# Optimization experiments

Hardware: AMD Instinct MI355X
Metric: run time of the kernel (lower is better)

Reference implementation:

```python
import jax, jax.numpy as jnp
import numpy as np

B, L, D_MODEL = 2, 2048, 2048
N_HEADS, N_GROUPS = 16, 4
D_HEAD = D_MODEL // N_HEADS  # 128
H_DIM = 5632
EPS = 1e-6


def rmsnorm(x, g):
    var = jnp.mean(x * x, axis=-1, keepdims=True)
    return x * jax.lax.rsqrt(var + EPS) * g


def apply_rope(x):
    # x: [b, H, l, d_head]; interleaved even/odd rotation as in the source
    l, d_head = x.shape[2], x.shape[3]
    pos = jnp.arange(l, dtype=jnp.float32)[:, None]                      # [l,1]
    div = 10000.0 ** (jnp.arange(0, d_head, 2, dtype=jnp.float32) / d_head)
    cos_e = jnp.cos(pos / div)                                           # [l, d_head//2]
    sin_e = jnp.sin(pos / div)
    xe, xo = x[..., 0::2], x[..., 1::2]
    re = xe * cos_e - xo * sin_e
    ro = xe * sin_e + xo * cos_e
    return jnp.stack([re, ro], axis=-1).reshape(x.shape)


def gqa_attention(q, k, v):
    # q: [b,l,d_model], k/v: [b,l,n_groups*d_head]
    b, l, _ = q.shape
    # faithful to source: direct contiguous view, NO transpose
    q = q.reshape(b, N_HEADS, l, D_HEAD)
    k = k.reshape(b, N_GROUPS, l, D_HEAD)
    v = v.reshape(b, N_GROUPS, l, D_HEAD)
    q = apply_rope(q)
    k = apply_rope(k)
    hpg = N_HEADS // N_GROUPS
    qg = q.reshape(b, N_GROUPS, hpg, l, D_HEAD)
    scale = 1.0 / jnp.sqrt(jnp.asarray(D_HEAD, dtype=q.dtype))
    scores = jnp.einsum('bghqd,bgkd->bghqk', qg, k) * scale              # [b,g,hpg,l,l]
    causal = jnp.tril(jnp.ones((l, l), dtype=bool))
    scores = jnp.where(causal, scores, jnp.asarray(-jnp.inf, scores.dtype))
    p = jax.nn.softmax(scores, axis=-1)
    out = jnp.einsum('bghqk,bgkd->bghqd', p, v)                          # [b,g,hpg,l,d]
    return out.reshape(b, N_HEADS, l, D_HEAD).reshape(b, l, D_MODEL)


def setup_inputs() -> dict:
    key = jax.random.key(0)
    ks = jax.random.split(key, 10)
    s_d = 1.0 / np.sqrt(D_MODEL)
    s_h = 1.0 / np.sqrt(H_DIM)
    return {
        'x': jax.random.normal(ks[0], (B, L, D_MODEL), jnp.float32),
        'g1': jnp.ones((D_MODEL,), jnp.float32),
        'wq': jax.random.normal(ks[1], (D_MODEL, D_MODEL), jnp.float32) * s_d,
        'bq': jnp.zeros((D_MODEL,), jnp.float32),
        'wk': jax.random.normal(ks[2], (D_MODEL, N_GROUPS * D_HEAD), jnp.float32) * s_d,
        'bk': jnp.zeros((N_GROUPS * D_HEAD,), jnp.float32),
        'wv': jax.random.normal(ks[3], (D_MODEL, N_GROUPS * D_HEAD), jnp.float32) * s_d,
        'bv': jnp.zeros((N_GROUPS * D_HEAD,), jnp.float32),
        'wo': jax.random.normal(ks[4], (D_MODEL, D_MODEL), jnp.float32) * s_d,
        'bo': jnp.zeros((D_MODEL,), jnp.float32),
        'g2': jnp.ones((D_MODEL,), jnp.float32),
        'w1': jax.random.normal(ks[5], (D_MODEL, H_DIM), jnp.float32) * s_d,
        'b1': jnp.zeros((H_DIM,), jnp.float32),
        'wg': jax.random.normal(ks[6], (D_MODEL, H_DIM), jnp.float32) * s_d,
        'bg': jnp.zeros((H_DIM,), jnp.float32),
        'w2': jax.random.normal(ks[7], (H_DIM, D_MODEL), jnp.float32) * s_h,
        'b2': jnp.zeros((D_MODEL,), jnp.float32),
    }


def reference(x, g1, wq, bq, wk, bk, wv, bv, wo, bo, g2, w1, b1, wg, bg, w2, b2):
    # pre-norm GQA attention block
    h = rmsnorm(x, g1)
    q = h @ wq + bq
    k = h @ wk + bk
    v = h @ wv + bv
    attn = gqa_attention(q, k, v)
    x = x + attn @ wo + bo
    # pre-norm SwiGLU FFN
    h2 = rmsnorm(x, g2)
    ffn = (jax.nn.silu(h2 @ w1 + b1) * (h2 @ wg + bg)) @ w2 + b2
    return x + ffn
```

## Files before the change

### kernel.cpp

```cpp
#include <hip/hip_runtime.h>
#include <math.h>

#define BATCH 2
#define SEQ 2048
#define DM 2048
#define NH 16
#define NG 4
#define DH 128
#define HDIM 5632
#define MROWS (BATCH * SEQ)
#define KVD (NG * DH)

typedef __attribute__((ext_vector_type(8))) short short8;
typedef __attribute__((ext_vector_type(4))) float f32x4;
typedef __attribute__((ext_vector_type(4))) unsigned short us4;
typedef unsigned short ushortT;

__device__ __forceinline__ unsigned short f2bf(float x) {
  unsigned int u = __float_as_uint(x);
  u += 0x7FFFu + ((u >> 16) & 1u);
  return (unsigned short)(u >> 16);
}
__device__ __forceinline__ float bf2f(unsigned short h) {
  return __uint_as_float(((unsigned int)h) << 16);
}

__global__ __launch_bounds__(256) void rmsnorm_planes(
    const float* __restrict__ x, const float* __restrict__ g,
    ushortT* __restrict__ Ah, ushortT* __restrict__ Al) {
  int row = blockIdx.x;
  const float4* xr = (const float4*)(x + (size_t)row * DM);
  const float4* g4 = (const float4*)g;
  int t = threadIdx.x;
  float4 a = xr[t];
  float4 b = xr[t + 256];
  float ss = a.x * a.x + a.y * a.y + a.z * a.z + a.w * a.w +
             b.x * b.x + b.y * b.y + b.z * b.z + b.w * b.w;
#pragma unroll
  for (int off = 32; off > 0; off >>= 1) ss += __shfl_xor(ss, off);
  __shared__ float red[4];
  if ((t & 63) == 0) red[t >> 6] = ss;
  __syncthreads();
  float tot = red[0] + red[1] + red[2] + red[3];
  float inv = rsqrtf(tot * (1.0f / DM) + 1e-6f);
  float4 ga = g4[t], gb = g4[t + 256];
  float va[4] = {a.x * inv * ga.x, a.y * inv * ga.y, a.z * inv * ga.z,
                 a.w * inv * ga.w};
  float vb[4] = {b.x * inv * gb.x, b.y * inv * gb.y, b.z * inv * gb.z,
                 b.w * inv * gb.w};
  us4 ha, la, hb, lb;
#pragma unroll
  for (int i = 0; i < 4; i++) {
    ushortT h = f2bf(va[i]);
    ha[i] = h; la[i] = f2bf(va[i] - bf2f(h));
    h = f2bf(vb[i]);
    hb[i] = h; lb[i] = f2bf(vb[i] - bf2f(h));
  }
  size_t o = (size_t)row * DM + 4 * t;
  *(us4*)&Ah[o] = ha; *(us4*)&Al[o] = la;
  *(us4*)&Ah[o + 1024] = hb; *(us4*)&Al[o + 1024] = lb;
}

__global__ __launch_bounds__(256) void split_wt(
    const float* __restrict__ W, ushortT* __restrict__ Wth,
    ushortT* __restrict__ Wtl, int K, int N) {
  __shared__ float Ls[64][65];
  int t = threadIdx.x;
  int nb = blockIdx.x * 64, kb = blockIdx.y * 64;
  int lr = t >> 4, lc = (t & 15) * 4;
#pragma unroll
  for (int r = 0; r < 4; r++) {
    float4 v = *(const float4*)&W[(size_t)(kb + lr + r * 16) * N + nb + lc];
    Ls[lr + r * 16][lc + 0] = v.x;
    Ls[lr + r * 16][lc + 1] = v.y;
    Ls[lr + r * 16][lc + 2] = v.z;
    Ls[lr + r * 16][lc + 3] = v.w;
  }
  __syncthreads();
  int nr = t >> 2, kc = (t & 3) * 16;
  ushortT hv[16], lv[16];
#pragma unroll
  for (int i = 0; i < 16; i++) {
    float v = Ls[kc + i][nr];
    hv[i] = f2bf(v);
    lv[i] = f2bf(v - bf2f(hv[i]));
  }
  size_t o = (size_t)(nb + nr) * K + kb + kc;
  *(uint4*)&Wth[o] = *(uint4*)&hv[0];
  *(uint4*)&Wth[o + 8] = *(uint4*)&hv[8];
  *(uint4*)&Wtl[o] = *(uint4*)&lv[0];
  *(uint4*)&Wtl[o + 8] = *(uint4*)&lv[8];
}

template <int EPI>
__global__ __launch_bounds__(256) void gemm_pl(
    const ushortT* __restrict__ Ah, const ushortT* __restrict__ Al,
    const ushortT* __restrict__ Wth, const ushortT* __restrict__ Wtl,
    const float* __restrict__ bias, const float* __restrict__ auxf,
    const ushortT* __restrict__ auxh, const ushortT* __restrict__ auxl,
    float* __restrict__ Cf, ushortT* __restrict__ Ch,
    ushortT* __restrict__ Cl, int M, int N, int K) {
  __shared__ ushortT As[2][128][40];
  __shared__ ushortT Bs[2][128][40];
  int t = threadIdx.x;
  int lane = t & 63, wid = t >> 6;
  int wr = wid >> 1, wc = wid & 1;
  int row0 = blockIdx.y * 128, col0 = blockIdx.x * 128;

  f32x4 acc[4][4];
#pragma unroll
  for (int mi = 0; mi < 4; mi++)
#pragma unroll
    for (int ni = 0; ni < 4; ni++)
#pragma unroll
      for (int j = 0; j < 4; j++) acc[mi][ni][j] = 0.f;

  int am = t >> 1, ak = (t & 1) * 16;
  int bn = t & 127, bk = (t >> 7) * 16;
  int fr = lane & 15, fq = lane >> 4;
  int fk = fq * 8;

  const ushortT* a0 = Ah + (size_t)(row0 + am) * K + ak;
  const ushortT* a1 = Al + (size_t)(row0 + am) * K + ak;
  const ushortT* b0 = Wth + (size_t)(col0 + bn) * K + bk;
  const ushortT* b1 = Wtl + (size_t)(col0 + bn) * K + bk;

  uint4 ra0 = *(const uint4*)(a0), ra1 = *(const uint4*)(a0 + 8);
  uint4 ra2 = *(const uint4*)(a1), ra3 = *(const uint4*)(a1 + 8);
  uint4 rb0 = *(const uint4*)(b0), rb1 = *(const uint4*)(b0 + 8);
  uint4 rb2 = *(const uint4*)(b1), rb3 = *(const uint4*)(b1 + 8);

  for (int k0 = 0; k0 < K; k0 += 32) {
    __syncthreads();
    *(uint4*)&As[0][am][ak + 0] = ra0;
    *(uint4*)&As[0][am][ak + 8] = ra1;
    *(uint4*)&As[1][am][ak + 0] = ra2;
    *(uint4*)&As[1][am][ak + 8] = ra3;
    *(uint4*)&Bs[0][bn][bk + 0] = rb0;
    *(uint4*)&Bs[0][bn][bk + 8] = rb1;
    *(uint4*)&Bs[1][bn][bk + 0] = rb2;
    *(uint4*)&Bs[1][bn][bk + 8] = rb3;
    __syncthreads();

    if (k0 + 32 < K) {
      ra0 = *(const uint4*)(a0 + k0 + 32);
      ra1 = *(const uint4*)(a0 + k0 + 40);
      ra2 = *(const uint4*)(a1 + k0 + 32);
      ra3 = *(const uint4*)(a1 + k0 + 40);
      rb0 = *(const uint4*)(b0 + k0 + 32);
      rb1 = *(const uint4*)(b0 + k0 + 40);
      rb2 = *(const uint4*)(b1 + k0 + 32);
      rb3 = *(const uint4*)(b1 + k0 + 40);
    }

    short8 bfr[4][2];
#pragma unroll
    for (int ni = 0; ni < 4; ni++) {
      int brow = wc * 64 + ni * 16 + fr;
      bfr[ni][0] = *(const short8*)&Bs[0][brow][fk];
      bfr[ni][1] = *(const short8*)&Bs[1][brow][fk];
    }
#pragma unroll
    for (int mi = 0; mi < 4; mi++) {
      int arow = wr * 64 + mi * 16 + fr;
      short8 a_h = *(const short8*)&As[0][arow][fk];
      short8 a_l = *(const short8*)&As[1][arow][fk];
#pragma unroll
      for (int ni = 0; ni < 4; ni++) {
        acc[mi][ni] = __builtin_amdgcn_mfma_f32_16x16x32_bf16(
            a_h, bfr[ni][0], acc[mi][ni], 0, 0, 0);
        acc[mi][ni] = __builtin_amdgcn_mfma_f32_16x16x32_bf16(
            a_h, bfr[ni][1], acc[mi][ni], 0, 0, 0);
        acc[mi][ni] = __builtin_amdgcn_mfma_f32_16x16x32_bf16(
            a_l, bfr[ni][0], acc[mi][ni], 0, 0, 0);
      }
    }
  }

#pragma unroll
  for (int mi = 0; mi < 4; mi++) {
#pragma unroll
    for (int ni = 0; ni < 4; ni++) {
      int row = row0 + wr * 64 + mi * 16 + fq * 4;
      int col = col0 + wc * 64 + ni * 16 + fr;
      float bc = bias[col];
#pragma unroll
      for (int j = 0; j < 4; j++) {
        size_t idx = (size_t)(row + j) * N + col;
        float v = acc[mi][ni][j] + bc;
        if (EPI == 1) v += auxf[idx];
        if (EPI == 3) {
          float u = bf2f(auxh[idx]) + bf2f(auxl[idx]);
          v = v * (u / (1.f + expf(-u)));
        }
        if (EPI <= 1) {
          Cf[idx] = v;
        } else {
          ushortT h = f2bf(v);
          Ch[idx] = h;
          Cl[idx] = f2bf(v - bf2f(h));
        }
      }
    }
  }
}

__global__ __launch_bounds__(256) void rope_table_kernel(float* __restrict__ tab) {
  int idx = blockIdx.x * 256 + threadIdx.x;
  if (idx >= SEQ * 64) return;
  int l = idx >> 6, i = idx & 63;
  double div = pow(10000.0, (double)(2 * i) / (double)DH);
  double ang = (double)l / div;
  tab[idx * 2 + 0] = (float)cos(ang);
  tab[idx * 2 + 1] = (float)sin(ang);
}

__global__ __launch_bounds__(256) void gather_rope_q_bf(
    const float* __restrict__ qmat, const float* __restrict__ tab,
    ushortT* __restrict__ Qh, ushortT* __restrict__ Ql) {
  int gid = blockIdx.x * 4 + (threadIdx.x >> 6);
  int lane = threadIdx.x & 63;
  int b = gid >> 15;
  int rem = gid & 32767;
  int h = rem >> 11, l2 = rem & 2047;
  int srow = h * 128 + (l2 >> 4);
  int scol = (l2 & 15) * 128;
  const float2* src = (const float2*)(qmat + ((size_t)b * SEQ + srow) * DM + scol);
  float2 v = src[lane];
  float2 cs = ((const float2*)tab)[l2 * 64 + lane];
  const float scale = (float)(0.08838834764831845 * 1.4426950408889634);
  float ox = (v.x * cs.x - v.y * cs.y) * scale;
  float oy = (v.x * cs.y + v.y * cs.x) * scale;
  ushortT hx = f2bf(ox), hy = f2bf(oy);
  ushortT lx = f2bf(ox - bf2f(hx)), ly = f2bf(oy - bf2f(hy));
  size_t o = (size_t)gid * DH + 2 * lane;
  Qh[o] = hx; Qh[o + 1] = hy;
  Ql[o] = lx; Ql[o + 1] = ly;
}

__global__ __launch_bounds__(256) void gather_k_bf(
    const float* __restrict__ mat, const float* __restrict__ tab,
    ushortT* __restrict__ Kh, ushortT* __restrict__ Kl) {
  int gid = blockIdx.x * 4 + (threadIdx.x >> 6);
  int lane = threadIdx.x & 63;
  int b = gid >> 13;
  int rem = gid & 8191;
  int g = rem >> 11, l2 = rem & 2047;
  int srow = g * 512 + (l2 >> 2);
  int scol = (l2 & 3) * 128;
  const float2* src = (const float2*)(mat + ((size_t)b * SEQ + srow) * KVD + scol);
  float2 v = src[lane];
  float2 cs = ((const float2*)tab)[l2 * 64 + lane];
  float ox = v.x * cs.x - v.y * cs.y;
  float oy = v.x * cs.y + v.y * cs.x;
  ushortT hx = f2bf(ox), hy = f2bf(oy);
  ushortT lx = f2bf(ox - bf2f(hx)), ly = f2bf(oy - bf2f(hy));
  size_t o = (size_t)gid * DH + 2 * lane;
  Kh[o] = hx; Kh[o + 1] = hy;
  Kl[o] = lx; Kl[o + 1] = ly;
}

__global__ __launch_bounds__(256) void gather_vt_bf(
    const float* __restrict__ vmat, ushortT* __restrict__ Vth,
    ushortT* __restrict__ Vtl) {
  __shared__ float Ls[64][33];
  int t = threadIdx.x;
  int bg = blockIdx.z;
  int b = bg >> 2, g = bg & 3;
  int l2base = blockIdx.x * 64, dbase = blockIdx.y * 32;
  int l2 = l2base + (t >> 2);
  int srow = g * 512 + (l2 >> 2);
  int scol = (l2 & 3) * 128 + dbase + (t & 3) * 8;
  const float* src = vmat + ((size_t)b * SEQ + srow) * KVD + scol;
  float4 v0 = *(const float4*)src;
  float4 v1 = *(const float4*)(src + 4);
  int lr = t >> 2, lc = (t & 3) * 8;
  Ls[lr][lc + 0] = v0.x; Ls[lr][lc + 1] = v0.y;
  Ls[lr][lc + 2] = v0.z; Ls[lr][lc + 3] = v0.w;
  Ls[lr][lc + 4] = v1.x; Ls[lr][lc + 5] = v1.y;
  Ls[lr][lc + 6] = v1.z; Ls[lr][lc + 7] = v1.w;
  __syncthreads();
  short8 hv, lv;
#pragma unroll
  for (int i = 0; i < 8; i++) {
    float v = Ls[(t & 7) * 8 + i][t >> 3];
    unsigned short h = f2bf(v);
    hv[i] = (short)h;
    lv[i] = (short)f2bf(v - bf2f(h));
  }
  size_t o = ((size_t)bg * DH + dbase + (t >> 3)) * SEQ + l2base + (t & 7) * 8;
  *(short8*)(Vth + o) = hv;
  *(short8*)(Vtl + o) = lv;
}

__global__ __launch_bounds__(256) void attn_mfma(
    const ushortT* __restrict__ Qh, const ushortT* __restrict__ Ql,
    const ushortT* __restrict__ Kh, const ushortT* __restrict__ Kl,
    const ushortT* __restrict__ Vth, const ushortT* __restrict__ Vtl,
    float* __restrict__ O) {
  __shared__ ushortT Ks[2][32][136];
  __shared__ ushortT Vts[2][128][40];
  __shared__ ushortT Ps[4][16][40];
  int t = threadIdx.x;
  int lane = t & 63, w = t >> 6;
  int fr = lane & 15, fq = lane >> 4;
  int bh = blockIdx.y;
  int bg = (bh >> 4) * NG + ((bh & 15) >> 2);
  int q0 = ((int)gridDim.x - 1 - (int)blockIdx.x) * 64;

  short8 qfh[4], qfl[4];
  {
    const ushortT* qs = Qh + ((size_t)bh * SEQ + q0 + w * 16 + fr) * DH + fq * 8;
    const ushortT* qs2 = Ql + ((size_t)bh * SEQ + q0 + w * 16 + fr) * DH + fq * 8;
#pragma unroll
    for (int ks = 0; ks < 4; ks++) {
      qfh[ks] = *(const short8*)(qs + ks * 32);
      qfl[ks] = *(const short8*)(qs2 + ks * 32);
    }
  }

  f32x4 oacc[8];
#pragma unroll
  for (int nt = 0; nt < 8; nt++)
#pragma unroll
    for (int j = 0; j < 4; j++) oacc[nt][j] = 0.f;
  float m[4], l[4];
#pragma unroll
  for (int j = 0; j < 4; j++) { m[j] = -INFINITY; l[j] = 0.f; }

  int nkt = q0 / 32 + 2;
  for (int kt = 0; kt < nkt; kt++) {
    int p = t >> 7, tt = t & 127;
    int kr = tt >> 2, cb = (tt & 3) * 32;
    const ushortT* ksp =
        (p ? Kl : Kh) + ((size_t)bg * SEQ + kt * 32 + kr) * DH + cb;
    uint4 k0 = *(const uint4*)(ksp + 0), k1 = *(const uint4*)(ksp + 8);
    uint4 k2 = *(const uint4*)(ksp + 16), k3 = *(const uint4*)(ksp + 24);
    const ushortT* vsp = (p ? Vtl : Vth) + ((size_t)bg * DH + tt) * SEQ + kt * 32;
    uint4 v0 = *(const uint4*)(vsp + 0), v1 = *(const uint4*)(vsp + 8);
    uint4 v2 = *(const uint4*)(vsp + 16), v3 = *(const uint4*)(vsp + 24);

    __syncthreads();
    *(uint4*)&Ks[p][kr][cb + 0] = k0;
    *(uint4*)&Ks[p][kr][cb + 8] = k1;
    *(uint4*)&Ks[p][kr][cb + 16] = k2;
    *(uint4*)&Ks[p][kr][cb + 24] = k3;
    int xs = (tt & 3) << 3;
    *(uint4*)&Vts[p][tt][0 ^ xs] = v0;
    *(uint4*)&Vts[p][tt][8 ^ xs] = v1;
    *(uint4*)&Vts[p][tt][16 ^ xs] = v2;
    *(uint4*)&Vts[p][tt][24 ^ xs] = v3;
    __syncthreads();

    f32x4 sc[2];
#pragma unroll
    for (int ct = 0; ct < 2; ct++)
#pragma unroll
      for (int j = 0; j < 4; j++) sc[ct][j] = 0.f;
#pragma unroll
    for (int ct = 0; ct < 2; ct++)
#pragma unroll
      for (int ks = 0; ks < 4; ks++) {
        short8 kfh = *(const short8*)&Ks[0][ct * 16 + fr][ks * 32 + fq * 8];
        short8 kfl = *(const short8*)&Ks[1][ct * 16 + fr][ks * 32 + fq * 8];
        sc[ct] = __builtin_amdgcn_mfma_f32_16x16x32_bf16(qfh[ks], kfh, sc[ct], 0, 0, 0);
        sc[ct] = __builtin_amdgcn_mfma_f32_16x16x32_bf16(qfh[ks], kfl, sc[ct], 0, 0, 0);
        sc[ct] = __builtin_amdgcn_mfma_f32_16x16x32_bf16(qfl[ks], kfh, sc[ct], 0, 0, 0);
      }

    float alpha[4];
#pragma unroll
    for (int j = 0; j < 4; j++) {
      int qg = q0 + w * 16 + fq * 4 + j;
      float s0 = (kt * 32 + fr <= qg) ? sc[0][j] : -INFINITY;
      float s1 = (kt * 32 + 16 + fr <= qg) ? sc[1][j] : -INFINITY;
      float mx = fmaxf(s0, s1);
      mx = fmaxf(mx, __shfl_xor(mx, 1));
      mx = fmaxf(mx, __shfl_xor(mx, 2));
      mx = fmaxf(mx, __shfl_xor(mx, 4));
      mx = fmaxf(mx, __shfl_xor(mx, 8));
      float mn = fmaxf(m[j], mx);
      float al = exp2f(m[j] - mn);
      float p0 = exp2f(s0 - mn), p1 = exp2f(s1 - mn);
      float rs = p0 + p1;
      rs += __shfl_xor(rs, 1);
      rs += __shfl_xor(rs, 2);
      rs += __shfl_xor(rs, 4);
      rs += __shfl_xor(rs, 8);
      l[j] = l[j] * al + rs;
      m[j] = mn;
      alpha[j] = al;
      Ps[w][fq * 4 + j][fr] = f2bf(p0);
      Ps[w][fq * 4 + j][16 + fr] = f2bf(p1);
    }
#pragma unroll
    for (int nt = 0; nt < 8; nt++) {
      oacc[nt][0] *= alpha[0];
      oacc[nt][1] *= alpha[1];
      oacc[nt][2] *= alpha[2];
      oacc[nt][3] *= alpha[3];
    }

    short8 pah = *(const short8*)&Ps[w][fr][fq * 8];
#pragma unroll
    for (int nt = 0; nt < 8; nt++) {
      int vr = nt * 16 + fr;
      int vc = (fq * 8) ^ ((fr & 3) << 3);
      short8 vfh = *(const short8*)&Vts[0][vr][vc];
      short8 vfl = *(const short8*)&Vts[1][vr][vc];
      oacc[nt] = __builtin_amdgcn_mfma_f32_16x16x32_bf16(pah, vfh, oacc[nt], 0, 0, 0);
      oacc[nt] = __builtin_amdgcn_mfma_f32_16x16x32_bf16(pah, vfl, oacc[nt], 0, 0, 0);
    }
  }

  float inv[4];
#pragma unroll
  for (int j = 0; j < 4; j++) inv[j] = 1.f / l[j];
  float* ob = O + ((size_t)bh * SEQ + q0 + w * 16 + fq * 4) * DH + fr;
#pragma unroll
  for (int nt = 0; nt < 8; nt++)
#pragma unroll
    for (int j = 0; j < 4; j++)
      ob[(size_t)j * DH + nt * 16] = oacc[nt][j] * inv[j];
}

__global__ __launch_bounds__(256) void scatter_o_planes(
    const float* __restrict__ O, ushortT* __restrict__ Sh,
    ushortT* __restrict__ Sl) {
  size_t i4 = (size_t)blockIdx.x * 256 + threadIdx.x;
  size_t f = i4 * 4;
  int b = (int)(f >> 22);
  int rem = (int)(f & 4194303);
  int l = rem >> 11, d = rem & 2047;
  int c = l * 16 + (d >> 7);
  int h = c >> 11, l2 = c & 2047, d2 = d & 127;
  float4 v = *(const float4*)&O[(((size_t)b * NH + h) * SEQ + l2) * DH + d2];
  float vv[4] = {v.x, v.y, v.z, v.w};
  us4 hv, lv;
#pragma unroll
  for (int i = 0; i < 4; i++) {
    ushortT h16 = f2bf(vv[i]);
    hv[i] = h16;
    lv[i] = f2bf(vv[i] - bf2f(h16));
  }
  *(us4*)&Sh[f] = hv;
  *(us4*)&Sl[f] = lv;
}

extern "C" void kernel_launch(void* const* d_in, const int* in_sizes, int n_in,
                              void* d_out, int out_size, void* d_ws,
                              size_t ws_size, hipStream_t stream) {
  if (ws_size < 53739520ull * 4ull) return;

  const float* x  = (const float*)d_in[0];
  const float* g1 = (const float*)d_in[1];
  const float* wq = (const float*)d_in[2];
  const float* bq = (const float*)d_in[3];
  const float* wk = (const float*)d_in[4];
  const float* bk = (const float*)d_in[5];
  const float* wv = (const float*)d_in[6];
  const float* bv = (const float*)d_in[7];
  const float* wo = (const float*)d_in[8];
  const float* bo = (const float*)d_in[9];
  const float* g2 = (const float*)d_in[10];
  const float* w1 = (const float*)d_in[11];
  const float* b1 = (const float*)d_in[12];
  const float* wg = (const float*)d_in[13];
  const float* bg = (const float*)d_in[14];
  const float* w2 = (const float*)d_in[15];
  const float* b2 = (const float*)d_in[16];
  float* out = (float*)d_out;
  float* ws = (float*)d_ws;

  ushortT* WTh = (ushortT*)(ws + 0);
  ushortT* Hh  = (ushortT*)(ws + 11534336);
  ushortT* Hl  = Hh + 8388608;
  float* qmat  = ws + 19922944;
  float* kmat  = ws + 28311552;
  float* vmat  = ws + 30408704;
  ushortT* Qh  = (ushortT*)(ws + 32505856);
  ushortT* Ql  = Qh + 8388608;
  ushortT* Kh  = (ushortT*)(ws + 40894464);
  ushortT* Kl  = Kh + 2097152;
  ushortT* Vth = (ushortT*)(ws + 42991616);
  ushortT* Vtl = Vth + 2097152;
  float* x2    = ws + 45088768;
  float* tab   = ws + 53477376;
  float* O     = qmat;
  ushortT* Sh  = Qh;
  ushortT* Sl  = Sh + 8388608;
  ushortT* Uh  = (ushortT*)qmat;
  ushortT* Ul  = Uh + 23068672;

  rope_table_kernel<<<(SEQ * 64 + 255) / 256, 256, 0, stream>>>(tab);
  rmsnorm_planes<<<MROWS, 256, 0, stream>>>(x, g1, Hh, Hl);

  split_wt<<<dim3(DM / 64, DM / 64), 256, 0, stream>>>(wq, WTh, WTh + DM * DM, DM, DM);
  gemm_pl<0><<<dim3(DM / 128, MROWS / 128), 256, 0, stream>>>(
      Hh, Hl, WTh, WTh + DM * DM, bq, nullptr, nullptr, nullptr, qmat, nullptr,
      nullptr, MROWS, DM, DM);
  split_wt<<<dim3(KVD / 64, DM / 64), 256, 0, stream>>>(wk, WTh, WTh + DM * KVD, DM, KVD);
  gemm_pl<0><<<dim3(KVD / 128, MROWS / 128), 256, 0, stream>>>(
      Hh, Hl, WTh, WTh + DM * KVD, bk, nullptr, nullptr, nullptr, kmat, nullptr,
      nullptr, MROWS, KVD, DM);
  split_wt<<<dim3(KVD / 64, DM / 64), 256, 0, stream>>>(wv, WTh, WTh + DM * KVD, DM, KVD);
  gemm_pl<0><<<dim3(KVD / 128, MROWS / 128), 256, 0, stream>>>(
      Hh, Hl, WTh, WTh + DM * KVD, bv, nullptr, nullptr, nullptr, vmat, nullptr,
      nullptr, MROWS, KVD, DM);

  gather_rope_q_bf<<<(BATCH * NH * SEQ) / 4, 256, 0, stream>>>(qmat, tab, Qh, Ql);
  gather_k_bf<<<(BATCH * NG * SEQ) / 4, 256, 0, stream>>>(kmat, tab, Kh, Kl);
  gather_vt_bf<<<dim3(SEQ / 64, DH / 32, BATCH * NG), 256, 0, stream>>>(vmat, Vth, Vtl);

  attn_mfma<<<dim3(SEQ / 64, BATCH * NH), 256, 0, stream>>>(Qh, Ql, Kh, Kl,
                                                            Vth, Vtl, O);
  scatter_o_planes<<<(MROWS * DM / 4) / 256, 256, 0, stream>>>(O, Sh, Sl);

  split_wt<<<dim3(DM / 64, DM / 64), 256, 0, stream>>>(wo, WTh, WTh + DM * DM, DM, DM);
  gemm_pl<1><<<dim3(DM / 128, MROWS / 128), 256, 0, stream>>>(
      Sh, Sl, WTh, WTh + DM * DM, bo, x, nullptr, nullptr, x2, nullptr,
      nullptr, MROWS, DM, DM);

  rmsnorm_planes<<<MROWS, 256, 0, stream>>>(x2, g2, Hh, Hl);

  split_wt<<<dim3(HDIM / 64, DM / 64), 256, 0, stream>>>(w1, WTh, WTh + DM * HDIM, DM, HDIM);
  gemm_pl<2><<<dim3(HDIM / 128, MROWS / 128), 256, 0, stream>>>(
      Hh, Hl, WTh, WTh + DM * HDIM, b1, nullptr, nullptr, nullptr, nullptr, Uh,
      Ul, MROWS, HDIM, DM);
  split_wt<<<dim3(HDIM / 64, DM / 64), 256, 0, stream>>>(wg, WTh, WTh + DM * HDIM, DM, HDIM);
  gemm_pl<3><<<dim3(HDIM / 128, MROWS / 128), 256, 0, stream>>>(
      Hh, Hl, WTh, WTh + DM * HDIM, bg, nullptr, Uh, Ul, nullptr, Uh, Ul,
      MROWS, HDIM, DM);

  split_wt<<<dim3(DM / 64, HDIM / 64), 256, 0, stream>>>(w2, WTh, WTh + HDIM * DM, HDIM, DM);
  gemm_pl<1><<<dim3(DM / 128, MROWS / 128), 256, 0, stream>>>(
      Uh, Ul, WTh, WTh + HDIM * DM, b2, x2, nullptr, nullptr, out, nullptr,
      nullptr, MROWS, DM, HDIM);
}
```

Baseline: 2.026 ms.

## Fuse QKV projections, merge SwiGLU GEMMs, prefetch K/V tiles in attention

The three Q/K/V projection GEMMs become one GEMM over concatenated transposed weights and a concatenated bias, and the gather kernels read from the combined output. The two FFN up and gate GEMMs become a single 512-thread kernel that computes both accumulators per tile and applies SiLU-gating in its epilogue. This avoids writing and rereading the intermediate U planes and saves several launches. The attention loop now loads the next K/V tile into registers while the current tile is in use, and the residual x2 is kept in the output buffer. In exchange the workspace grows, register pressure rises in the dual GEMM and in attention, and the final residual add reads and writes the same buffer in place.

```diff
diff --git a/kernel.cpp b/kernel.cpp
--- a/kernel.cpp
+++ b/kernel.cpp
@@ -10,6 +10,7 @@
 #define HDIM 5632
 #define MROWS (BATCH * SEQ)
 #define KVD (NG * DH)
+#define QKVD 3072
 
 typedef __attribute__((ext_vector_type(8))) short short8;
 typedef __attribute__((ext_vector_type(4))) float f32x4;
@@ -92,14 +93,20 @@
   *(uint4*)&Wtl[o + 8] = *(uint4*)&lv[8];
 }
 
+__global__ __launch_bounds__(256) void bias_cat(
+    const float* __restrict__ bq, const float* __restrict__ bk,
+    const float* __restrict__ bv, float* __restrict__ dst) {
+  int t = blockIdx.x * 256 + threadIdx.x;
+  if (t >= QKVD) return;
+  dst[t] = (t < DM) ? bq[t] : ((t < DM + KVD) ? bk[t - DM] : bv[t - DM - KVD]);
+}
+
 template <int EPI>
 __global__ __launch_bounds__(256) void gemm_pl(
     const ushortT* __restrict__ Ah, const ushortT* __restrict__ Al,
     const ushortT* __restrict__ Wth, const ushortT* __restrict__ Wtl,
     const float* __restrict__ bias, const float* __restrict__ auxf,
-    const ushortT* __restrict__ auxh, const ushortT* __restrict__ auxl,
-    float* __restrict__ Cf, ushortT* __restrict__ Ch,
-    ushortT* __restrict__ Cl, int M, int N, int K) {
+    float* __restrict__ Cf, int M, int N, int K) {
   __shared__ ushortT As[2][128][40];
   __shared__ ushortT Bs[2][128][40];
   int t = threadIdx.x;
@@ -189,17 +196,114 @@
         size_t idx = (size_t)(row + j) * N + col;
         float v = acc[mi][ni][j] + bc;
         if (EPI == 1) v += auxf[idx];
-        if (EPI == 3) {
-          float u = bf2f(auxh[idx]) + bf2f(auxl[idx]);
-          v = v * (u / (1.f + expf(-u)));
-        }
-        if (EPI <= 1) {
-          Cf[idx] = v;
-        } else {
-          ushortT h = f2bf(v);
-          Ch[idx] = h;
-          Cl[idx] = f2bf(v - bf2f(h));
-        }
+        Cf[idx] = v;
+      }
+    }
+  }
+}
+
+__global__ __launch_bounds__(512) void gemm_dual(
+    const ushortT* __restrict__ Ah, const ushortT* __restrict__ Al,
+    const ushortT* __restrict__ W1h, const ushortT* __restrict__ W1l,
+    const ushortT* __restrict__ W2h, const ushortT* __restrict__ W2l,
+    const float* __restrict__ b1, const float* __restrict__ bg,
+    ushortT* __restrict__ Mh, ushortT* __restrict__ Ml, int M, int N, int K) {
+  __shared__ ushortT As[2][128][40];
+  __shared__ ushortT B1s[2][128][40];
+  __shared__ ushortT B2s[2][128][40];
+  int t = threadIdx.x;
+  int lane = t & 63, wid = t >> 6;
+  int wr = wid >> 2, wc = wid & 3;
+  int row0 = blockIdx.y * 128, col0 = blockIdx.x * 128;
+
+  f32x4 accu[4][2], accg[4][2];
+#pragma unroll
+  for (int mi = 0; mi < 4; mi++)
+#pragma unroll
+    for (int ni = 0; ni < 2; ni++)
+#pragma unroll
+      for (int j = 0; j < 4; j++) { accu[mi][ni][j] = 0.f; accg[mi][ni][j] = 0.f; }
+
+  int p = t >> 8, tt = t & 255;
+  int am = tt >> 1, ak = (tt & 1) * 16;
+  int fr = lane & 15, fq = lane >> 4;
+  int fk = fq * 8;
+
+  const ushortT* ap = (p ? Al : Ah) + (size_t)(row0 + am) * K + ak;
+  const ushortT* b1p = (p ? W1l : W1h) + (size_t)(col0 + am) * K + ak;
+  const ushortT* b2p = (p ? W2l : W2h) + (size_t)(col0 + am) * K + ak;
+
+  uint4 ra0 = *(const uint4*)(ap), ra1 = *(const uint4*)(ap + 8);
+  uint4 rb0 = *(const uint4*)(b1p), rb1 = *(const uint4*)(b1p + 8);
+  uint4 rc0 = *(const uint4*)(b2p), rc1 = *(const uint4*)(b2p + 8);
+
+  for (int k0 = 0; k0 < K; k0 += 32) {
+    __syncthreads();
+    *(uint4*)&As[p][am][ak + 0] = ra0;
+    *(uint4*)&As[p][am][ak + 8] = ra1;
+    *(uint4*)&B1s[p][am][ak + 0] = rb0;
+    *(uint4*)&B1s[p][am][ak + 8] = rb1;
+    *(uint4*)&B2s[p][am][ak + 0] = rc0;
+    *(uint4*)&B2s[p][am][ak + 8] = rc1;
+    __syncthreads();
+
+    if (k0 + 32 < K) {
+      ra0 = *(const uint4*)(ap + k0 + 32);
+      ra1 = *(const uint4*)(ap + k0 + 40);
+      rb0 = *(const uint4*)(b1p + k0 + 32);
+      rb1 = *(const uint4*)(b1p + k0 + 40);
+      rc0 = *(const uint4*)(b2p + k0 + 32);
+      rc1 = *(const uint4*)(b2p + k0 + 40);
+    }
+
+    short8 b1f[2][2], b2f[2][2];
+#pragma unroll
+    for (int ni = 0; ni < 2; ni++) {
+      int brow = wc * 32 + ni * 16 + fr;
+      b1f[ni][0] = *(const short8*)&B1s[0][brow][fk];
+      b1f[ni][1] = *(const short8*)&B1s[1][brow][fk];
+      b2f[ni][0] = *(const short8*)&B2s[0][brow][fk];
+      b2f[ni][1] = *(const short8*)&B2s[1][brow][fk];
+    }
+#pragma unroll
+    for (int mi = 0; mi < 4; mi++) {
+      int arow = wr * 64 + mi * 16 + fr;
+      short8 a_h = *(const short8*)&As[0][arow][fk];
+      short8 a_l = *(const short8*)&As[1][arow][fk];
+#pragma unroll
+      for (int ni = 0; ni < 2; ni++) {
+        accu[mi][ni] = __builtin_amdgcn_mfma_f32_16x16x32_bf16(
+            a_h, b1f[ni][0], accu[mi][ni], 0, 0, 0);
+        accu[mi][ni] = __builtin_amdgcn_mfma_f32_16x16x32_bf16(
+            a_h, b1f[ni][1], accu[mi][ni], 0, 0, 0);
+        accu[mi][ni] = __builtin_amdgcn_mfma_f32_16x16x32_bf16(
+            a_l, b1f[ni][0], accu[mi][ni], 0, 0, 0);
+        accg[mi][ni] = __builtin_amdgcn_mfma_f32_16x16x32_bf16(
+            a_h, b2f[ni][0], accg[mi][ni], 0, 0, 0);
+        accg[mi][ni] = __builtin_amdgcn_mfma_f32_16x16x32_bf16(
+            a_h, b2f[ni][1], accg[mi][ni], 0, 0, 0);
+        accg[mi][ni] = __builtin_amdgcn_mfma_f32_16x16x32_bf16(
+            a_l, b2f[ni][0], accg[mi][ni], 0, 0, 0);
+      }
+    }
+  }
+
+#pragma unroll
+  for (int mi = 0; mi < 4; mi++) {
+#pragma unroll
+    for (int ni = 0; ni < 2; ni++) {
+      int row = row0 + wr * 64 + mi * 16 + fq * 4;
+      int col = col0 + wc * 32 + ni * 16 + fr;
+      float b1c = b1[col], bgc = bg[col];
+#pragma unroll
+      for (int j = 0; j < 4; j++) {
+        size_t idx = (size_t)(row + j) * N + col;
+        float u = accu[mi][ni][j] + b1c;
+        float g = accg[mi][ni][j] + bgc;
+        float v = (u / (1.f + expf(-u))) * g;
+        ushortT h = f2bf(v);
+        Mh[idx] = h;
+        Ml[idx] = f2bf(v - bf2f(h));
       }
     }
   }
@@ -216,7 +320,7 @@
 }
 
 __global__ __launch_bounds__(256) void gather_rope_q_bf(
-    const float* __restrict__ qmat, const float* __restrict__ tab,
+    const float* __restrict__ qkv, const float* __restrict__ tab,
     ushortT* __restrict__ Qh, ushortT* __restrict__ Ql) {
   int gid = blockIdx.x * 4 + (threadIdx.x >> 6);
   int lane = threadIdx.x & 63;
@@ -225,7 +329,8 @@
   int h = rem >> 11, l2 = rem & 2047;
   int srow = h * 128 + (l2 >> 4);
   int scol = (l2 & 15) * 128;
-  const float2* src = (const float2*)(qmat + ((size_t)b * SEQ + srow) * DM + scol);
+  const float2* src =
+      (const float2*)(qkv + ((size_t)b * SEQ + srow) * QKVD + scol);
   float2 v = src[lane];
   float2 cs = ((const float2*)tab)[l2 * 64 + lane];
   const float scale = (float)(0.08838834764831845 * 1.4426950408889634);
@@ -239,7 +344,7 @@
 }
 
 __global__ __launch_bounds__(256) void gather_k_bf(
-    const float* __restrict__ mat, const float* __restrict__ tab,
+    const float* __restrict__ qkv, const float* __restrict__ tab,
     ushortT* __restrict__ Kh, ushortT* __restrict__ Kl) {
   int gid = blockIdx.x * 4 + (threadIdx.x >> 6);
   int lane = threadIdx.x & 63;
@@ -248,7 +353,8 @@
   int g = rem >> 11, l2 = rem & 2047;
   int srow = g * 512 + (l2 >> 2);
   int scol = (l2 & 3) * 128;
-  const float2* src = (const float2*)(mat + ((size_t)b * SEQ + srow) * KVD + scol);
+  const float2* src =
+      (const float2*)(qkv + ((size_t)b * SEQ + srow) * QKVD + DM + scol);
   float2 v = src[lane];
   float2 cs = ((const float2*)tab)[l2 * 64 + lane];
   float ox = v.x * cs.x - v.y * cs.y;
@@ -261,7 +367,7 @@
 }
 
 __global__ __launch_bounds__(256) void gather_vt_bf(
-    const float* __restrict__ vmat, ushortT* __restrict__ Vth,
+    const float* __restrict__ qkv, ushortT* __restrict__ Vth,
     ushortT* __restrict__ Vtl) {
   __shared__ float Ls[64][33];
   int t = threadIdx.x;
@@ -271,7 +377,7 @@
   int l2 = l2base + (t >> 2);
   int srow = g * 512 + (l2 >> 2);
   int scol = (l2 & 3) * 128 + dbase + (t & 3) * 8;
-  const float* src = vmat + ((size_t)b * SEQ + srow) * KVD + scol;
+  const float* src = qkv + ((size_t)b * SEQ + srow) * QKVD + DM + KVD + scol;
   float4 v0 = *(const float4*)src;
   float4 v1 = *(const float4*)(src + 4);
   int lr = t >> 2, lc = (t & 3) * 8;
@@ -328,29 +434,38 @@
 #pragma unroll
   for (int j = 0; j < 4; j++) { m[j] = -INFINITY; l[j] = 0.f; }
 
+  int p = t >> 7, tt = t & 127;
+  int kr = tt >> 2, cb = (tt & 3) * 32;
+  const ushortT* kbase = (p ? Kl : Kh) + ((size_t)bg * SEQ + kr) * DH + cb;
+  const ushortT* vbase = (p ? Vtl : Vth) + ((size_t)bg * DH + tt) * SEQ;
+  int xs = (tt & 3) << 3;
+
+  uint4 rk0 = *(const uint4*)(kbase + 0), rk1 = *(const uint4*)(kbase + 8);
+  uint4 rk2 = *(const uint4*)(kbase + 16), rk3 = *(const uint4*)(kbase + 24);
+  uint4 rv0 = *(const uint4*)(vbase + 0), rv1 = *(const uint4*)(vbase + 8);
+  uint4 rv2 = *(const uint4*)(vbase + 16), rv3 = *(const uint4*)(vbase + 24);
+
   int nkt = q0 / 32 + 2;
   for (int kt = 0; kt < nkt; kt++) {
-    int p = t >> 7, tt = t & 127;
-    int kr = tt >> 2, cb = (tt & 3) * 32;
-    const ushortT* ksp =
-        (p ? Kl : Kh) + ((size_t)bg * SEQ + kt * 32 + kr) * DH + cb;
-    uint4 k0 = *(const uint4*)(ksp + 0), k1 = *(const uint4*)(ksp + 8);
-    uint4 k2 = *(const uint4*)(ksp + 16), k3 = *(const uint4*)(ksp + 24);
-    const ushortT* vsp = (p ? Vtl : Vth) + ((size_t)bg * DH + tt) * SEQ + kt * 32;
-    uint4 v0 = *(const uint4*)(vsp + 0), v1 = *(const uint4*)(vsp + 8);
-    uint4 v2 = *(const uint4*)(vsp + 16), v3 = *(const uint4*)(vsp + 24);
-
     __syncthreads();
-    *(uint4*)&Ks[p][kr][cb + 0] = k0;
-    *(uint4*)&Ks[p][kr][cb + 8] = k1;
-    *(uint4*)&Ks[p][kr][cb + 16] = k2;
-    *(uint4*)&Ks[p][kr][cb + 24] = k3;
-    int xs = (tt & 3) << 3;
-    *(uint4*)&Vts[p][tt][0 ^ xs] = v0;
-    *(uint4*)&Vts[p][tt][8 ^ xs] = v1;
-    *(uint4*)&Vts[p][tt][16 ^ xs] = v2;
-    *(uint4*)&Vts[p][tt][24 ^ xs] = v3;
+    *(uint4*)&Ks[p][kr][cb + 0] = rk0;
+    *(uint4*)&Ks[p][kr][cb + 8] = rk1;
+    *(uint4*)&Ks[p][kr][cb + 16] = rk2;
+    *(uint4*)&Ks[p][kr][cb + 24] = rk3;
+    *(uint4*)&Vts[p][tt][0 ^ xs] = rv0;
+    *(uint4*)&Vts[p][tt][8 ^ xs] = rv1;
+    *(uint4*)&Vts[p][tt][16 ^ xs] = rv2;
+    *(uint4*)&Vts[p][tt][24 ^ xs] = rv3;
     __syncthreads();
+
+    if (kt + 1 < nkt) {
+      const ushortT* kp = kbase + (size_t)(kt + 1) * 32 * DH;
+      const ushortT* vp = vbase + (kt + 1) * 32;
+      rk0 = *(const uint4*)(kp + 0);  rk1 = *(const uint4*)(kp + 8);
+      rk2 = *(const uint4*)(kp + 16); rk3 = *(const uint4*)(kp + 24);
+      rv0 = *(const uint4*)(vp + 0);  rv1 = *(const uint4*)(vp + 8);
+      rv2 = *(const uint4*)(vp + 16); rv3 = *(const uint4*)(vp + 24);
+    }
 
     f32x4 sc[2];
 #pragma unroll
@@ -450,7 +565,7 @@
 extern "C" void kernel_launch(void* const* d_in, const int* in_sizes, int n_in,
                               void* d_out, int out_size, void* d_ws,
                               size_t ws_size, hipStream_t stream) {
-  if (ws_size < 53739520ull * 4ull) return;
+  if (ws_size < 56885248ull * 4ull) return;
 
   const float* x  = (const float*)d_in[0];
   const float* g1 = (const float*)d_in[1];
@@ -472,68 +587,68 @@
   float* out = (float*)d_out;
   float* ws = (float*)d_ws;
 
-  ushortT* WTh = (ushortT*)(ws + 0);
-  ushortT* Hh  = (ushortT*)(ws + 11534336);
-  ushortT* Hl  = Hh + 8388608;
-  float* qmat  = ws + 19922944;
-  float* kmat  = ws + 28311552;
-  float* vmat  = ws + 30408704;
-  ushortT* Qh  = (ushortT*)(ws + 32505856);
-  ushortT* Ql  = Qh + 8388608;
-  ushortT* Kh  = (ushortT*)(ws + 40894464);
-  ushortT* Kl  = Kh + 2097152;
-  ushortT* Vth = (ushortT*)(ws + 42991616);
-  ushortT* Vtl = Vth + 2097152;
-  float* x2    = ws + 45088768;
-  float* tab   = ws + 53477376;
-  float* O     = qmat;
-  ushortT* Sh  = Qh;
-  ushortT* Sl  = Sh + 8388608;
-  ushortT* Uh  = (ushortT*)qmat;
-  ushortT* Ul  = Uh + 23068672;
+  ushortT* WT1u = (ushortT*)(ws + 0);
+  float*   WT2f = ws + 11534336;
+  ushortT* WT2u = (ushortT*)WT2f;
+  ushortT* Hh   = (ushortT*)(ws + 23068672);
+  ushortT* Hl   = Hh + 8388608;
+  float*   qkv  = ws + 31457280;
+  ushortT* Qh   = (ushortT*)(ws + 44040192);
+  ushortT* Ql   = Qh + 8388608;
+  ushortT* Kh   = (ushortT*)(ws + 52428800);
+  ushortT* Kl   = Kh + 2097152;
+  ushortT* Vth  = (ushortT*)(ws + 54525952);
+  ushortT* Vtl  = Vth + 2097152;
+  float*   tab  = ws + 56623104;
+  float*   biasqkv = WT2f;
+  float*   O    = WT2f;
+  ushortT* Sh   = Qh;
+  ushortT* Sl   = Sh + 8388608;
+  ushortT* Mh   = (ushortT*)qkv;
+  ushortT* Ml   = Mh + 23068672;
 
   rope_table_kernel<<<(SEQ * 64 + 255) / 256, 256, 0, stream>>>(tab);
+  bias_cat<<<(QKVD + 255) / 256, 256, 0, stream>>>(bq, bk, bv, biasqkv);
   rmsnorm_planes<<<MROWS, 256, 0, stream>>>(x, g1, Hh, Hl);
 
-  split_wt<<<dim3(DM / 64, DM / 64), 256, 0, stream>>>(wq, WTh, WTh + DM * DM, DM, DM);
-  gemm_pl<0><<<dim3(DM / 128, MROWS / 128), 256, 0, stream>>>(
-      Hh, Hl, WTh, WTh + DM * DM, bq, nullptr, nullptr, nullptr, qmat, nullptr,
-      nullptr, MROWS, DM, DM);
-  split_wt<<<dim3(KVD / 64, DM / 64), 256, 0, stream>>>(wk, WTh, WTh + DM * KVD, DM, KVD);
-  gemm_pl<0><<<dim3(KVD / 128, MROWS / 128), 256, 0, stream>>>(
-      Hh, Hl, WTh, WTh + DM * KVD, bk, nullptr, nullptr, nullptr, kmat, nullptr,
-      nullptr, MROWS, KVD, DM);
-  split_wt<<<dim3(KVD / 64, DM / 64), 256, 0, stream>>>(wv, WTh, WTh + DM * KVD, DM, KVD);
-  gemm_pl<0><<<dim3(KVD / 128, MROWS / 128), 256, 0, stream>>>(
-      Hh, Hl, WTh, WTh + DM * KVD, bv, nullptr, nullptr, nullptr, vmat, nullptr,
-      nullptr, MROWS, KVD, DM);
-
-  gather_rope_q_bf<<<(BATCH * NH * SEQ) / 4, 256, 0, stream>>>(qmat, tab, Qh, Ql);
-  gather_k_bf<<<(BATCH * NG * SEQ) / 4, 256, 0, stream>>>(kmat, tab, Kh, Kl);
-  gather_vt_bf<<<dim3(SEQ / 64, DH / 32, BATCH * NG), 256, 0, stream>>>(vmat, Vth, Vtl);
+  split_wt<<<dim3(DM / 64, DM / 64), 256, 0, stream>>>(
+      wq, WT1u, WT1u + (size_t)QKVD * DM, DM, DM);
+  split_wt<<<dim3(KVD / 64, DM / 64), 256, 0, stream>>>(
+      wk, WT1u + (size_t)DM * DM, WT1u + (size_t)QKVD * DM + (size_t)DM * DM,
+      DM, KVD);
+  split_wt<<<dim3(KVD / 64, DM / 64), 256, 0, stream>>>(
+      wv, WT1u + (size_t)(DM + KVD) * DM,
+      WT1u + (size_t)QKVD * DM + (size_t)(DM + KVD) * DM, DM, KVD);
+  gemm_pl<0><<<dim3(QKVD / 128, MROWS / 128), 256, 0, stream>>>(
+      Hh, Hl, WT1u, WT1u + (size_t)QKVD * DM, biasqkv, nullptr, qkv, MROWS,
+      QKVD, DM);
+
+  gather_rope_q_bf<<<(BATCH * NH * SEQ) / 4, 256, 0, stream>>>(qkv, tab, Qh, Ql);
+  gather_k_bf<<<(BATCH * NG * SEQ) / 4, 256, 0, stream>>>(qkv, tab, Kh, Kl);
+  gather_vt_bf<<<dim3(SEQ / 64, DH / 32, BATCH * NG), 256, 0, stream>>>(
+      qkv, Vth, Vtl);
 
   attn_mfma<<<dim3(SEQ / 64, BATCH * NH), 256, 0, stream>>>(Qh, Ql, Kh, Kl,
                                                             Vth, Vtl, O);
   scatter_o_planes<<<(MROWS * DM / 4) / 256, 256, 0, stream>>>(O, Sh, Sl);
 
-  split_wt<<<dim3(DM / 64, DM / 64), 256, 0, stream>>>(wo, WTh, WTh + DM * DM, DM, DM);
+  split_wt<<<dim3(DM / 64, DM / 64), 256, 0, stream>>>(
+      wo, WT1u, WT1u + (size_t)DM * DM, DM, DM);
   gemm_pl<1><<<dim3(DM / 128, MROWS / 128), 256, 0, stream>>>(
-      Sh, Sl, WTh, WTh + DM * DM, bo, x, nullptr, nullptr, x2, nullptr,
-      nullptr, MROWS, DM, DM);
-
-  rmsnorm_planes<<<MROWS, 256, 0, stream>>>(x2, g2, Hh, Hl);
-
-  split_wt<<<dim3(HDIM / 64, DM / 64), 256, 0, stream>>>(w1, WTh, WTh + DM * HDIM, DM, HDIM);
-  gemm_pl<2><<<dim3(HDIM / 128, MROWS / 128), 256, 0, stream>>>(
-      Hh, Hl, WTh, WTh + DM * HDIM, b1, nullptr, nullptr, nullptr, nullptr, Uh,
-      Ul, MROWS, HDIM, DM);
-  split_wt<<<dim3(HDIM / 64, DM / 64), 256, 0, stream>>>(wg, WTh, WTh + DM * HDIM, DM, HDIM);
-  gemm_pl<3><<<dim3(HDIM / 128, MROWS / 128), 256, 0, stream>>>(
-      Hh, Hl, WTh, WTh + DM * HDIM, bg, nullptr, Uh, Ul, nullptr, Uh, Ul,
-      MROWS, HDIM, DM);
-
-  split_wt<<<dim3(DM / 64, HDIM / 64), 256, 0, stream>>>(w2, WTh, WTh + HDIM * DM, HDIM, DM);
+      Sh, Sl, WT1u, WT1u + (size_t)DM * DM, bo, x, out, MROWS, DM, DM);
+
+  rmsnorm_planes<<<MROWS, 256, 0, stream>>>(out, g2, Hh, Hl);
+
+  split_wt<<<dim3(HDIM / 64, DM / 64), 256, 0, stream>>>(
+      w1, WT1u, WT1u + (size_t)HDIM * DM, DM, HDIM);
+  split_wt<<<dim3(HDIM / 64, DM / 64), 256, 0, stream>>>(
+      wg, WT2u, WT2u + (size_t)HDIM * DM, DM, HDIM);
+  gemm_dual<<<dim3(HDIM / 128, MROWS / 128), 512, 0, stream>>>(
+      Hh, Hl, WT1u, WT1u + (size_t)HDIM * DM, WT2u, WT2u + (size_t)HDIM * DM,
+      b1, bg, Mh, Ml, MROWS, HDIM, DM);
+
+  split_wt<<<dim3(DM / 64, HDIM / 64), 256, 0, stream>>>(
+      w2, WT1u, WT1u + (size_t)DM * HDIM, HDIM, DM);
   gemm_pl<1><<<dim3(DM / 128, MROWS / 128), 256, 0, stream>>>(
-      Uh, Ul, WTh, WTh + HDIM * DM, b2, x2, nullptr, nullptr, out, nullptr,
-      nullptr, MROWS, DM, HDIM);
-}
+      Mh, Ml, WT1u, WT1u + (size_t)DM * HDIM, b2, out, out, MROWS, DM, HDIM);
+}
```

Result: faster. 1.854 ms (-8.5%).
